# Optimization experiments

Measured on AMD Instinct MI355X. Metric: run time of the kernel, lower is better.

## Reference

```python
import jax, jax.numpy as jnp
import numpy as np
from collections import deque

N, IN_DIM, H, B, L = 512, 64, 128, 256, 2
SOURCE = 105
E_UND = 2048


def _build_graph_and_masks():
    rng = np.random.default_rng(0)
    s = rng.integers(0, N, E_UND)
    d = rng.integers(0, N, E_UND)
    edge_index = np.stack([np.concatenate([s, d]), np.concatenate([d, s])]).astype(np.int32)
    # BFS depths from source (undirected)
    adj = [[] for _ in range(N)]
    for a, b in zip(edge_index[0], edge_index[1]):
        adj[int(a)].append(int(b))
    depths = np.full(N, np.inf)
    depths[SOURCE] = 0.0
    q = deque([SOURCE]); seen = {SOURCE}
    while q:
        u = q.popleft()
        for v in adj[u]:
            if v not in seen:
                seen.add(v); depths[v] = depths[u] + 1.0; q.append(v)
    finite = np.isfinite(depths)
    maxd = depths[finite].max() if finite.any() else 0.0
    depths[~finite] = maxd + 1.0
    adj_mask = np.zeros((N, N), np.float32)
    adj_mask[edge_index[0], edge_index[1]] = 1.0
    adj_mask[edge_index[1], edge_index[0]] = 1.0
    np.fill_diagonal(adj_mask, 1.0)
    direction_mask = (depths[None, :] <= depths[:, None]).astype(np.float32)
    # admittance_matrix is None -> uniform init, then masked
    initial_causal = (np.ones((N, N), np.float32) / N) * adj_mask * direction_mask
    return edge_index, adj_mask, direction_mask, initial_causal


def setup_inputs() -> dict:
    key = jax.random.key(0)
    ks = jax.random.split(key, 16)
    edge_index, adj_mask, direction_mask, initial_causal = _build_graph_and_masks()
    w = lambda k, shp: jax.random.normal(k, shp, jnp.float32) * 0.02
    return {
        'x': jax.random.normal(ks[0], (B, N, IN_DIM), jnp.float32),
        'edge_index': jnp.asarray(edge_index),
        'adj_mask': jnp.asarray(adj_mask),
        'direction_mask': jnp.asarray(direction_mask),
        'causal_logits': jnp.asarray(initial_causal),  # nn.Parameter init
        'W_in': w(ks[1], (IN_DIM, H)), 'b_in': jnp.zeros((H,), jnp.float32),
        'Wq': w(ks[2], (H, H)), 'bq': jnp.zeros((H,), jnp.float32),
        'Wk': w(ks[3], (H, H)), 'bk': jnp.zeros((H,), jnp.float32),
        'Wv': w(ks[4], (H, H)), 'bv': jnp.zeros((H,), jnp.float32),
        'gcn_W': w(ks[5], (L, H, H)), 'gcn_b': jnp.zeros((L, H), jnp.float32),
        'W_fuse': w(ks[6], (2 * H, H)), 'b_fuse': jnp.zeros((H,), jnp.float32),
        'ln_g': jnp.ones((H,), jnp.float32), 'ln_b': jnp.zeros((H,), jnp.float32),
    }


def reference(x, edge_index, adj_mask, direction_mask, causal_logits,
              W_in, b_in, Wq, bq, Wk, bk, Wv, bv,
              gcn_W, gcn_b, W_fuse, b_fuse, ln_g, ln_b):
    n = adj_mask.shape[0]
    h = jax.nn.relu(x @ W_in + b_in)                               # (B,N,H)

    # causal matrix: softmax over learned logits, physically masked, renormalized
    C = jax.nn.softmax(causal_logits, axis=-1) * adj_mask * direction_mask
    C = C / jnp.clip(C.sum(-1, keepdims=True), 1e-8)

    # masked causal attention
    Q = h @ Wq + bq; K = h @ Wk + bk; V = h @ Wv + bv
    scale = jnp.asarray(h.shape[-1] ** 0.5, h.dtype)
    attn = jax.nn.softmax(jnp.einsum('bnh,bmh->bnm', Q, K) / scale, axis=-1)
    attn = attn * C[None]
    attn = attn / (attn.sum(-1, keepdims=True) + 1e-8)
    h_causal = jnp.einsum('bnm,bmh->bnh', attn, V)

    # GCNConv stack (self-loops + symmetric norm; dropout is identity in eval)
    src = jnp.concatenate([edge_index[0], jnp.arange(n, dtype=edge_index.dtype)])
    dst = jnp.concatenate([edge_index[1], jnp.arange(n, dtype=edge_index.dtype)])
    deg = jnp.zeros((n,), h.dtype).at[dst].add(1.0)
    dinv = deg ** -0.5                                              # deg>=1 (self loops)
    norm = (dinv[src] * dinv[dst])[None, :, None]                   # (1,E+N,1)
    h_g = h
    for l in range(gcn_W.shape[0]):
        hW = h_g @ gcn_W[l]                                         # (B,N,H)
        msg = hW[:, src, :] * norm                                  # (B,E+N,H)
        h_g = jnp.zeros_like(hW).at[:, dst, :].add(msg) + gcn_b[l]
        h_g = jax.nn.relu(h_g)

    h_comb = jnp.concatenate([h_causal, h_g], axis=-1) @ W_fuse + b_fuse
    mu = h_comb.mean(-1, keepdims=True)
    var = ((h_comb - mu) ** 2).mean(-1, keepdims=True)
    out = (h_comb - mu) / jnp.sqrt(var + 1e-5) * ln_g + ln_b
    return out, C
```

## Files before the change

### kernel.cpp

```cpp
#include <hip/hip_runtime.h>
#include <hip/hip_bf16.h>
#include <math.h>

#define NN 512
#define HH 128
#define INDIM 64
#define BB 256
#define NE 4096
#define MROWS (BB*NN)
#define OUT0 (BB*NN*HH)

typedef __attribute__((ext_vector_type(8))) short short8v;
typedef __attribute__((ext_vector_type(4))) float float4v;

__device__ __forceinline__ unsigned short f2bf(float f) {
  unsigned u = __float_as_uint(f);
  unsigned r = (u + 0x7fffu + ((u >> 16) & 1u)) >> 16;
  return (unsigned short)r;
}
__device__ __forceinline__ float bf2f(unsigned short b) {
  return __uint_as_float(((unsigned)b) << 16);
}

__global__ __launch_bounds__(256) void k_causalC(
    const float* __restrict__ logits, const float* __restrict__ adj,
    const float* __restrict__ dir, float* __restrict__ Cout)
{
  const int row = blockIdx.x;
  const int t = threadIdx.x;
  __shared__ float red[256];
  const float* lrow = logits + (size_t)row * NN;
  float v0 = lrow[t], v1 = lrow[t + 256];
  float mx = fmaxf(v0, v1);
  red[t] = mx; __syncthreads();
  for (int s = 128; s > 0; s >>= 1) { if (t < s) red[t] = fmaxf(red[t], red[t + s]); __syncthreads(); }
  mx = red[0]; __syncthreads();
  float e0 = __expf(v0 - mx), e1 = __expf(v1 - mx);
  red[t] = e0 + e1; __syncthreads();
  for (int s = 128; s > 0; s >>= 1) { if (t < s) red[t] += red[t + s]; __syncthreads(); }
  float sumE = red[0]; __syncthreads();
  float m0 = adj[(size_t)row * NN + t] * dir[(size_t)row * NN + t];
  float m1 = adj[(size_t)row * NN + t + 256] * dir[(size_t)row * NN + t + 256];
  float me0 = e0 * m0, me1 = e1 * m1;
  red[t] = me0 + me1; __syncthreads();
  for (int s = 128; s > 0; s >>= 1) { if (t < s) red[t] += red[t + s]; __syncthreads(); }
  float sumME = red[0];
  float sm = sumME / sumE;
  float denom = fmaxf(sm, 1e-8f) * sumE;
  Cout[(size_t)row * NN + t]       = me0 / denom;
  Cout[(size_t)row * NN + t + 256] = me1 / denom;
}

__global__ __launch_bounds__(512) void k_csr(const int* __restrict__ ei,
                                             int* __restrict__ rp,
                                             int* __restrict__ ci,
                                             float* __restrict__ cw)
{
  __shared__ int scnt[512];
  __shared__ float sdinv[512];
  __shared__ int sval[512];
  __shared__ int scur[512];
  const int t = threadIdx.x;
  const int* src = ei;
  const int* dst = ei + NE;
  scnt[t] = 0;
  __syncthreads();
  for (int e = t; e < NE; e += 512) atomicAdd(&scnt[dst[e]], 1);
  __syncthreads();
  const int deg = scnt[t] + 1;
  sdinv[t] = rsqrtf((float)deg);
  sval[t] = deg;
  __syncthreads();
  for (int off = 1; off < 512; off <<= 1) {
    int add = (t >= off) ? sval[t - off] : 0;
    __syncthreads();
    sval[t] += add;
    __syncthreads();
  }
  const int excl = sval[t] - deg;
  rp[t] = excl;
  if (t == 511) rp[512] = excl + deg;
  ci[excl] = t;
  cw[excl] = sdinv[t] * sdinv[t];
  scur[t] = excl + 1;
  __syncthreads();
  for (int e = t; e < NE; e += 512) {
    int s = src[e], d = dst[e];
    int p = atomicAdd(&scur[d], 1);
    ci[p] = s;
    cw[p] = sdinv[s] * sdinv[d];
  }
}

__global__ __launch_bounds__(512) void k_ccsr(const int* __restrict__ ei,
                                              const float* __restrict__ Cmat,
                                              int* __restrict__ rp,
                                              int* __restrict__ ci,
                                              float* __restrict__ cw)
{
  __shared__ unsigned bm[512 * 16];
  __shared__ int cnt[512];
  __shared__ int sval[512];
  __shared__ int cur[512];
  const int t = threadIdx.x;
  const int* src = ei;
  const int* dst = ei + NE;
  for (int i = t; i < 512 * 16; i += 512) bm[i] = 0u;
  __syncthreads();
  bm[t * 16 + (t >> 5)] |= (1u << (t & 31));
  cnt[t] = 1;
  __syncthreads();
  for (int e = t; e < NE; e += 512) {
    int r = src[e], c = dst[e];
    if (Cmat[(size_t)r * NN + c] > 0.f) {
      unsigned bit = 1u << (c & 31);
      unsigned old = atomicOr(&bm[r * 16 + (c >> 5)], bit);
      if (!(old & bit)) atomicAdd(&cnt[r], 1);
    }
  }
  __syncthreads();
  const int myc = cnt[t];
  sval[t] = myc;
  __syncthreads();
  for (int off = 1; off < 512; off <<= 1) {
    int add = (t >= off) ? sval[t - off] : 0;
    __syncthreads();
    sval[t] += add;
    __syncthreads();
  }
  const int excl = sval[t] - myc;
  rp[t] = excl;
  if (t == 511) rp[512] = excl + myc;
  ci[excl] = t;
  cw[excl] = Cmat[(size_t)t * NN + t];
  cur[t] = excl + 1;
  bm[t * 16 + (t >> 5)] &= ~(1u << (t & 31));
  __syncthreads();
  for (int e = t; e < NE; e += 512) {
    int r = src[e], c = dst[e];
    if (Cmat[(size_t)r * NN + c] > 0.f) {
      unsigned bit = 1u << (c & 31);
      unsigned old = atomicAnd(&bm[r * 16 + (c >> 5)], ~bit);
      if (old & bit) {
        int p = atomicAdd(&cur[r], 1);
        ci[p] = c;
        cw[p] = Cmat[(size_t)r * NN + c];
      }
    }
  }
}

__global__ __launch_bounds__(256) void k_gcn(
    const unsigned short* __restrict__ hW,
    const int* __restrict__ rp, const int* __restrict__ ci,
    const float* __restrict__ cw, const float* __restrict__ bias,
    unsigned short* __restrict__ out, int OS, int OC0)
{
  const int bid = blockIdx.x;
  const int i5 = bid >> 3;
  const int ng = i5 & 31;
  const int b = (bid & 7) * 32 + (i5 >> 5);
  const int t = threadIdx.x;
  const int node = ng * 16 + (t >> 4);
  const int f0 = (t & 15) * 8;

  float bcol[8];
  #pragma unroll
  for (int k = 0; k < 8; k++) bcol[k] = bias[f0 + k];

  const unsigned short* base = hW + (size_t)b * 512 * 128;
  const int beg = rp[node], end = rp[node + 1];
  float acc[8] = {0.f, 0.f, 0.f, 0.f, 0.f, 0.f, 0.f, 0.f};
  for (int j = beg; j < end; j++) {
    int s = ci[j];
    float w = cw[j];
    short8v v = *(const short8v*)&base[(size_t)s * 128 + f0];
    #pragma unroll
    for (int k = 0; k < 8; k++) acc[k] += w * bf2f((unsigned short)v[k]);
  }
  short8v o;
  #pragma unroll
  for (int k = 0; k < 8; k++) {
    float v = fmaxf(acc[k] + bcol[k], 0.f);
    o[k] = (short)f2bf(v);
  }
  *(short8v*)&out[((size_t)(b * 512 + node)) * OS + OC0 + f0] = o;
}

__global__ __launch_bounds__(256) void k_sattn(
    const unsigned short* __restrict__ Qbf, const unsigned short* __restrict__ Kbf,
    const unsigned short* __restrict__ Vbf,
    const int* __restrict__ rp, const int* __restrict__ ci,
    const float* __restrict__ cw,
    unsigned short* __restrict__ Ocb)
{
  const int bid = blockIdx.x;
  const int i5 = bid >> 3;
  const int ng = i5 & 31;
  const int b = (bid & 7) * 32 + (i5 >> 5);
  const int t = threadIdx.x;
  const int node = ng * 16 + (t >> 4);
  const int f0 = (t & 15) * 8;
  const float scale = 0.088388347648318447f;

  const size_t rowq = ((size_t)(b * 512 + node)) * 128 + f0;
  short8v qv = *(const short8v*)&Qbf[rowq];
  float qf[8];
  #pragma unroll
  for (int k = 0; k < 8; k++) qf[k] = bf2f((unsigned short)qv[k]);

  const unsigned short* Kb = Kbf + (size_t)b * 512 * 128;
  const unsigned short* Vb = Vbf + (size_t)b * 512 * 128;
  const int beg = rp[node], end = rp[node + 1];
  float acc[8] = {0.f, 0.f, 0.f, 0.f, 0.f, 0.f, 0.f, 0.f};
  float sw = 0.f;
  for (int j = beg; j < end; j++) {
    int m = ci[j];
    float w0 = cw[j];
    short8v kv = *(const short8v*)&Kb[(size_t)m * 128 + f0];
    short8v vv = *(const short8v*)&Vb[(size_t)m * 128 + f0];
    float part = 0.f;
    #pragma unroll
    for (int k = 0; k < 8; k++) part += qf[k] * bf2f((unsigned short)kv[k]);
    part += __shfl_xor(part, 1);
    part += __shfl_xor(part, 2);
    part += __shfl_xor(part, 4);
    part += __shfl_xor(part, 8);
    float w = __expf(part * scale) * w0;
    sw += w;
    #pragma unroll
    for (int k = 0; k < 8; k++) acc[k] += w * bf2f((unsigned short)vv[k]);
  }
  float inv = 1.0f / sw;
  short8v o;
  #pragma unroll
  for (int k = 0; k < 8; k++) o[k] = (short)f2bf(acc[k] * inv);
  *(short8v*)&Ocb[((size_t)(b * 512 + node)) * 256 + f0] = o;
}

__global__ __launch_bounds__(256) void k_wt(
    const float* s0, const float* s1, const float* s2, const float* s3,
    const float* s4, const float* s5, const float* s6,
    unsigned short* d0, unsigned short* d1, unsigned short* d2, unsigned short* d3,
    unsigned short* d4, unsigned short* d5, unsigned short* d6)
{
  const float* srcs[7] = {s0, s1, s2, s3, s4, s5, s6};
  unsigned short* dsts[7] = {d0, d1, d2, d3, d4, d5, d6};
  const int Ks[7] = {64, 128, 128, 128, 128, 128, 256};
  const int j = blockIdx.x >> 3;
  const int nc = blockIdx.x & 7;
  const float* s = srcs[j];
  unsigned short* d = dsts[j];
  const int K = Ks[j];
  const int STRW = K + 8;
  const int n0 = nc * 16;
  __shared__ short tile[16 * 264];
  const int t = threadIdx.x;
  for (int i = t; i < K * 16; i += 256) {
    int k = i >> 4, nn = i & 15;
    tile[nn * STRW + k] = (short)f2bf(s[k * 128 + n0 + nn]);
  }
  __syncthreads();
  for (int i = t; i < K * 2; i += 256) {
    int nn = (i * 8) / K;
    int k  = (i * 8) % K;
    *(short8v*)&d[(size_t)(n0 + nn) * K + k] =
        *(const short8v*)&tile[nn * STRW + k];
  }
}

#define GNT 4
template<int KD, bool RELU, bool BATCHW, int OMODE, bool AF32>
__global__ __launch_bounds__(256) void k_bgemm(
    const void* __restrict__ Ap, const unsigned short* __restrict__ Wt,
    const float* __restrict__ bias, void* __restrict__ Out, int OS,
    const float* __restrict__ lng, const float* __restrict__ lnb)
{
  constexpr int KCH = (KD < 128) ? KD : 128;
  constexpr int STR = KCH + 8;
  constexpr bool WONCE = (KD <= 128);
  constexpr int ASH = (64 * STR > 8192) ? 64 * STR : 8192;
  constexpr int TRIPS = KCH / 32;
  __shared__ short lds[ASH + 128 * STR];
  short* As = lds;
  short* Ws = lds + ASH;
  const unsigned short* Abf = (const unsigned short*)Ap;
  const float* Af = (const float*)Ap;
  const int t = threadIdx.x;
  const int wave = t >> 6, lane = t & 63;
  const int l15 = lane & 15, quad = lane >> 4;

  short8v ap[TRIPS];
  float4 fa[TRIPS], fb[TRIPS];

  auto LOADC = [&](int rb, int kc) {
    #pragma unroll
    for (int j = 0; j < TRIPS; j++) {
      int i = t + j * 256;
      int r = i / (KCH / 8), seg = i % (KCH / 8);
      if (AF32) {
        const float* sp = &Af[(size_t)(rb + r) * KD + kc + seg * 8];
        fa[j] = *(const float4*)sp;
        fb[j] = *(const float4*)(sp + 4);
      } else {
        int arow = BATCHW ? ((rb & 511) + r) : (rb + r);
        ap[j] = *(const short8v*)&Abf[(size_t)arow * KD + kc + seg * 8];
      }
    }
  };
  auto STOREC = [&]() {
    #pragma unroll
    for (int j = 0; j < TRIPS; j++) {
      int i = t + j * 256;
      int r = i / (KCH / 8), seg = i % (KCH / 8);
      if (AF32) {
        short8v pk;
        pk[0] = (short)f2bf(fa[j].x); pk[1] = (short)f2bf(fa[j].y);
        pk[2] = (short)f2bf(fa[j].z); pk[3] = (short)f2bf(fa[j].w);
        pk[4] = (short)f2bf(fb[j].x); pk[5] = (short)f2bf(fb[j].y);
        pk[6] = (short)f2bf(fb[j].z); pk[7] = (short)f2bf(fb[j].w);
        *(short8v*)&As[r * STR + seg * 8] = pk;
      } else {
        *(short8v*)&As[r * STR + seg * 8] = ap[j];
      }
    }
  };

  float bcol[8];
  #pragma unroll
  for (int nt = 0; nt < 8; nt++) bcol[nt] = bias ? bias[nt * 16 + l15] : 0.f;
  float gcol[8], bbcol[8];
  if (OMODE == 2) {
    #pragma unroll
    for (int nt = 0; nt < 8; nt++) { gcol[nt] = lng[nt * 16 + l15]; bbcol[nt] = lnb[nt * 16 + l15]; }
  }

  for (int g = blockIdx.x; g < (MROWS / 64) / GNT; g += gridDim.x) {
    if (WONCE) {
      const int b0 = (g * GNT * 64) >> 9;
      const unsigned short* Wb = BATCHW ? (Wt + (size_t)b0 * 128 * KD) : Wt;
      for (int i = t; i < 128 * (KCH / 8); i += 256) {
        int n = i / (KCH / 8), seg = i % (KCH / 8);
        *(short8v*)&Ws[n * STR + seg * 8] =
            *(const short8v*)&Wb[(size_t)n * KD + seg * 8];
      }
    }
    LOADC(g * GNT * 64, 0);
    for (int tt = 0; tt < GNT; tt++) {
      const int tile = g * GNT + tt;
      const int rowbase = tile * 64;
      const int b = rowbase >> 9;
      float4v acc[8];
      #pragma unroll
      for (int nt = 0; nt < 8; nt++) acc[nt] = (float4v){0.f, 0.f, 0.f, 0.f};

      for (int kc = 0; kc < KD; kc += KCH) {
        __syncthreads();
        STOREC();
        if (!WONCE) {
          const unsigned short* Wb = BATCHW ? (Wt + (size_t)b * 128 * KD) : Wt;
          for (int i = t; i < 128 * (KCH / 8); i += 256) {
            int n = i / (KCH / 8), seg = i % (KCH / 8);
            *(short8v*)&Ws[n * STR + seg * 8] =
                *(const short8v*)&Wb[(size_t)n * KD + kc + seg * 8];
          }
        }
        __syncthreads();
        {
          int nkc = kc + KCH, ntt = tt;
          if (nkc >= KD) { nkc = 0; ntt = tt + 1; }
          if (ntt < GNT) LOADC((g * GNT + ntt) * 64, nkc);
        }
        #pragma unroll
        for (int k32 = 0; k32 < KCH / 32; k32++) {
          short8v af = *(const short8v*)&As[(wave * 16 + l15) * STR + k32 * 32 + quad * 8];
          #pragma unroll
          for (int nt = 0; nt < 8; nt++) {
            short8v wf = *(const short8v*)&Ws[(nt * 16 + l15) * STR + k32 * 32 + quad * 8];
            acc[nt] = __builtin_amdgcn_mfma_f32_16x16x32_bf16(af, wf, acc[nt], 0, 0, 0);
          }
        }
      }

      __syncthreads();
      if (OMODE == 0) {
        short* rep = As + wave * 2048;
        #pragma unroll
        for (int nt = 0; nt < 8; nt++)
          #pragma unroll
          for (int r = 0; r < 4; r++) {
            float v = acc[nt][r] + bcol[nt];
            if (RELU) v = fmaxf(v, 0.f);
            rep[(quad * 4 + r) * 128 + nt * 16 + l15] = (short)f2bf(v);
          }
        __syncthreads();
        unsigned short* Ob = (unsigned short*)Out;
        #pragma unroll
        for (int p = 0; p < 4; p++) {
          int row16 = (lane >> 4) + p * 4, seg = lane & 15;
          short8v vv = *(const short8v*)&rep[row16 * 128 + seg * 8];
          *(short8v*)&Ob[(size_t)(rowbase + wave * 16 + row16) * OS + seg * 8] = vv;
        }
      } else if (OMODE == 1) {
        short* rep = As + wave * 2048;
        #pragma unroll
        for (int nt = 0; nt < 8; nt++)
          #pragma unroll
          for (int r = 0; r < 4; r++) {
            float v = acc[nt][r] + bcol[nt];
            if (RELU) v = fmaxf(v, 0.f);
            rep[(nt * 16 + l15) * 16 + quad * 4 + r] = (short)f2bf(v);
          }
        __syncthreads();
        unsigned short* Ob = (unsigned short*)Out;
        int node0 = (rowbase & 511) + wave * 16;
        #pragma unroll
        for (int p = 0; p < 4; p++) {
          int idx = p * 64 + lane, c = idx >> 1, half = idx & 1;
          short8v vv = *(const short8v*)&rep[c * 16 + half * 8];
          *(short8v*)&Ob[((size_t)(b * 128 + c)) * 512 + node0 + half * 8] = vv;
        }
      } else {
        float* repw = (float*)lds + wave * 2048;
        float vv[8][4];
        float s[4] = {0, 0, 0, 0}, ss[4] = {0, 0, 0, 0};
        #pragma unroll
        for (int nt = 0; nt < 8; nt++)
          #pragma unroll
          for (int r = 0; r < 4; r++) {
            float v = acc[nt][r] + bcol[nt];
            vv[nt][r] = v;
            s[r] += v; ss[r] += v * v;
          }
        #pragma unroll
        for (int r = 0; r < 4; r++) {
          s[r] += __shfl_xor(s[r], 1);  s[r] += __shfl_xor(s[r], 2);
          s[r] += __shfl_xor(s[r], 4);  s[r] += __shfl_xor(s[r], 8);
          ss[r] += __shfl_xor(ss[r], 1); ss[r] += __shfl_xor(ss[r], 2);
          ss[r] += __shfl_xor(ss[r], 4); ss[r] += __shfl_xor(ss[r], 8);
        }
        #pragma unroll
        for (int r = 0; r < 4; r++) {
          float mu = s[r] * (1.0f / 128.0f);
          float var = ss[r] * (1.0f / 128.0f) - mu * mu;
          float inv = rsqrtf(var + 1e-5f);
          #pragma unroll
          for (int nt = 0; nt < 8; nt++)
            repw[(quad * 4 + r) * 128 + nt * 16 + l15] =
                (vv[nt][r] - mu) * inv * gcol[nt] + bbcol[nt];
        }
        __syncthreads();
        float* Of = (float*)Out;
        #pragma unroll
        for (int p = 0; p < 8; p++) {
          int row16 = (lane >> 5) + p * 2, seg = lane & 31;
          float4 o = *(const float4*)&repw[row16 * 128 + seg * 4];
          *(float4*)&Of[(size_t)(rowbase + wave * 16 + row16) * 128 + seg * 4] = o;
        }
      }
    }
  }
}

__global__ __launch_bounds__(256) void k_qkv(
    const unsigned short* __restrict__ Abf,
    const unsigned short* __restrict__ W0, const unsigned short* __restrict__ W1,
    const unsigned short* __restrict__ W2,
    const float* __restrict__ b0, const float* __restrict__ b1,
    const float* __restrict__ b2,
    unsigned short* __restrict__ O0, unsigned short* __restrict__ O1,
    unsigned short* __restrict__ O2)
{
  constexpr int STR = 136;
  __shared__ short lds[8704 + 128 * STR];
  short* As = lds;
  short* Ws = lds + 8704;
  const int t = threadIdx.x;
  const int wave = t >> 6, lane = t & 63;
  const int l15 = lane & 15, quad = lane >> 4;

  const unsigned short* Wsrc[3] = {W0, W1, W2};
  const float* Bsrc[3] = {b0, b1, b2};
  unsigned short* Osrc[3] = {O0, O1, O2};

  short8v ap[4];
  auto LOADC = [&](int rb) {
    #pragma unroll
    for (int j = 0; j < 4; j++) {
      int i = t + j * 256;
      int r = i >> 4, seg = i & 15;
      ap[j] = *(const short8v*)&Abf[(size_t)(rb + r) * 128 + seg * 8];
    }
  };

  for (int g = blockIdx.x; g < (MROWS / 64) / GNT; g += gridDim.x) {
    #pragma unroll
    for (int s = 0; s < 3; s++) {
      for (int i = t; i < 128 * 16; i += 256) {
        int n = i >> 4, seg = i & 15;
        *(short8v*)&Ws[n * STR + seg * 8] =
            *(const short8v*)&Wsrc[s][(size_t)n * 128 + seg * 8];
      }
      float bcol[8];
      #pragma unroll
      for (int nt = 0; nt < 8; nt++) bcol[nt] = Bsrc[s][nt * 16 + l15];
      if (s == 0) LOADC(g * GNT * 64);

      for (int tt = 0; tt < GNT; tt++) {
        const int rowbase = (g * GNT + tt) * 64;
        float4v acc[8];
        #pragma unroll
        for (int nt = 0; nt < 8; nt++) acc[nt] = (float4v){0.f, 0.f, 0.f, 0.f};

        __syncthreads();
        #pragma unroll
        for (int j = 0; j < 4; j++) {
          int i = t + j * 256;
          int r = i >> 4, seg = i & 15;
          *(short8v*)&As[r * STR + seg * 8] = ap[j];
        }
        __syncthreads();

        {
          int ntt = tt + 1;
          if (ntt < GNT) LOADC((g * GNT + ntt) * 64);
          else if (s < 2) LOADC(g * GNT * 64);
        }

        #pragma unroll
        for (int k32 = 0; k32 < 4; k32++) {
          short8v af = *(const short8v*)&As[(wave * 16 + l15) * STR + k32 * 32 + quad * 8];
          #pragma unroll
          for (int nt = 0; nt < 8; nt++) {
            short8v wf = *(const short8v*)&Ws[(nt * 16 + l15) * STR + k32 * 32 + quad * 8];
            acc[nt] = __builtin_amdgcn_mfma_f32_16x16x32_bf16(af, wf, acc[nt], 0, 0, 0);
          }
        }
        __syncthreads();

        unsigned short* Ob = Osrc[s];
        short* rep = As + wave * 2048;
        #pragma unroll
        for (int nt = 0; nt < 8; nt++)
          #pragma unroll
          for (int r = 0; r < 4; r++) {
            float v = acc[nt][r] + bcol[nt];
            rep[(quad * 4 + r) * 128 + nt * 16 + l15] = (short)f2bf(v);
          }
        __syncthreads();
        #pragma unroll
        for (int p = 0; p < 4; p++) {
          int row16 = (lane >> 4) + p * 4, seg = lane & 15;
          short8v vv = *(const short8v*)&rep[row16 * 128 + seg * 8];
          *(short8v*)&Ob[(size_t)(rowbase + wave * 16 + row16) * 128 + seg * 8] = vv;
        }
      }
    }
  }
}

extern "C" void kernel_launch(void* const* d_in, const int* in_sizes, int n_in,
                              void* d_out, int out_size, void* d_ws, size_t ws_size,
                              hipStream_t stream)
{
  const float* x     = (const float*)d_in[0];
  const int*   ei    = (const int*)d_in[1];
  const float* adj   = (const float*)d_in[2];
  const float* dmask = (const float*)d_in[3];
  const float* clog  = (const float*)d_in[4];
  const float* W_in  = (const float*)d_in[5];
  const float* b_in  = (const float*)d_in[6];
  const float* Wq    = (const float*)d_in[7];
  const float* bq    = (const float*)d_in[8];
  const float* Wk    = (const float*)d_in[9];
  const float* bk    = (const float*)d_in[10];
  const float* Wv    = (const float*)d_in[11];
  const float* bv    = (const float*)d_in[12];
  const float* gcnW  = (const float*)d_in[13];
  const float* gcnB  = (const float*)d_in[14];
  const float* Wf    = (const float*)d_in[15];
  const float* bf    = (const float*)d_in[16];
  const float* lng   = (const float*)d_in[17];
  const float* lnb   = (const float*)d_in[18];

  float* outp = (float*)d_out;
  float* Cmat = outp + OUT0;

  char* W = (char*)d_ws;
  const size_t SLOT = (size_t)MROWS * 128 * 2;
  unsigned short* A0 = (unsigned short*)(W);
  unsigned short* B0 = (unsigned short*)(W + SLOT);
  unsigned short* C0 = (unsigned short*)(W + 2 * SLOT);
  unsigned short* D0 = (unsigned short*)(W + 3 * SLOT);
  char* AUX = W + 5 * SLOT;
  int*   csr_rp = (int*)AUX;
  int*   csr_ci = csr_rp + 640;
  float* csr_cw = (float*)(csr_ci + 4608);
  int*   crp    = (int*)(AUX + 131072);
  int*   cci    = crp + 640;
  float* ccw    = (float*)(cci + 8192);
  unsigned short* WB    = (unsigned short*)(AUX + 512 * 512 * 4) + 512 * 512 * 2;
  unsigned short* W_int = WB;
  unsigned short* Wqt   = WB + 8192;
  unsigned short* Wkt   = Wqt + 16384;
  unsigned short* Wvt   = Wkt + 16384;
  unsigned short* G0t   = Wvt + 16384;
  unsigned short* G1t   = G0t + 16384;
  unsigned short* Wft   = G1t + 16384;

  unsigned short* Vbf = (unsigned short*)outp;

  k_causalC<<<512, 256, 0, stream>>>(clog, adj, dmask, Cmat);
  k_csr<<<1, 512, 0, stream>>>(ei, csr_rp, csr_ci, csr_cw);
  k_ccsr<<<1, 512, 0, stream>>>(ei, Cmat, crp, cci, ccw);
  k_wt<<<56, 256, 0, stream>>>(W_in, Wq, Wk, Wv, gcnW, gcnW + HH * HH, Wf,
                               W_int, Wqt, Wkt, Wvt, G0t, G1t, Wft);

  k_bgemm<64, true, false, 0, true><<<512, 256, 0, stream>>>(
      x, W_int, b_in, B0, 128, nullptr, nullptr);
  k_bgemm<128, false, false, 0, false><<<512, 256, 0, stream>>>(
      B0, G0t, nullptr, C0, 128, nullptr, nullptr);
  k_gcn<<<8192, 256, 0, stream>>>(C0, csr_rp, csr_ci, csr_cw, gcnB, A0, 128, 0);
  k_bgemm<128, false, false, 0, false><<<512, 256, 0, stream>>>(
      A0, G1t, nullptr, C0, 128, nullptr, nullptr);
  k_gcn<<<8192, 256, 0, stream>>>(C0, csr_rp, csr_ci, csr_cw, gcnB + HH, D0, 256, 128);
  k_qkv<<<512, 256, 0, stream>>>(
      B0, Wqt, Wkt, Wvt, bq, bk, bv, C0, A0, Vbf);
  k_sattn<<<8192, 256, 0, stream>>>(C0, A0, Vbf, crp, cci, ccw, D0);
  k_bgemm<256, false, false, 2, false><<<512, 256, 0, stream>>>(
      D0, Wft, bf, outp, 128, lng, lnb);
}
```

Measured before the change: 388.7 us.

## Fuse GCN aggregation into GEMM by aggregating before transform, prefetch attention neighbors

Each GCN layer previously ran a GEMM followed by a separate sparse aggregation kernel. This uses linearity, A(hW) = (Ah)W, to gather and aggregate neighbor rows straight into LDS as the GEMM A-tile, then apply the MFMA transform with bias and ReLU. That removes one kernel launch and one intermediate round trip per layer. Separately, the sparse attention and the new gather loop software-prefetch the next neighbor's K/V rows. The trade-off is an extra bf16 rounding of the aggregated input, and irregular gathers inside the GEMM kernel may stall the MFMA phase.

After: 566.1 us. 45.7% more time.

```diff
diff --git a/kernel.cpp b/kernel.cpp
--- a/kernel.cpp
+++ b/kernel.cpp
@@ -150,43 +150,6 @@
   }
 }
 
-__global__ __launch_bounds__(256) void k_gcn(
-    const unsigned short* __restrict__ hW,
-    const int* __restrict__ rp, const int* __restrict__ ci,
-    const float* __restrict__ cw, const float* __restrict__ bias,
-    unsigned short* __restrict__ out, int OS, int OC0)
-{
-  const int bid = blockIdx.x;
-  const int i5 = bid >> 3;
-  const int ng = i5 & 31;
-  const int b = (bid & 7) * 32 + (i5 >> 5);
-  const int t = threadIdx.x;
-  const int node = ng * 16 + (t >> 4);
-  const int f0 = (t & 15) * 8;
-
-  float bcol[8];
-  #pragma unroll
-  for (int k = 0; k < 8; k++) bcol[k] = bias[f0 + k];
-
-  const unsigned short* base = hW + (size_t)b * 512 * 128;
-  const int beg = rp[node], end = rp[node + 1];
-  float acc[8] = {0.f, 0.f, 0.f, 0.f, 0.f, 0.f, 0.f, 0.f};
-  for (int j = beg; j < end; j++) {
-    int s = ci[j];
-    float w = cw[j];
-    short8v v = *(const short8v*)&base[(size_t)s * 128 + f0];
-    #pragma unroll
-    for (int k = 0; k < 8; k++) acc[k] += w * bf2f((unsigned short)v[k]);
-  }
-  short8v o;
-  #pragma unroll
-  for (int k = 0; k < 8; k++) {
-    float v = fmaxf(acc[k] + bcol[k], 0.f);
-    o[k] = (short)f2bf(v);
-  }
-  *(short8v*)&out[((size_t)(b * 512 + node)) * OS + OC0 + f0] = o;
-}
-
 __global__ __launch_bounds__(256) void k_sattn(
     const unsigned short* __restrict__ Qbf, const unsigned short* __restrict__ Kbf,
     const unsigned short* __restrict__ Vbf,
@@ -214,11 +177,17 @@
   const int beg = rp[node], end = rp[node + 1];
   float acc[8] = {0.f, 0.f, 0.f, 0.f, 0.f, 0.f, 0.f, 0.f};
   float sw = 0.f;
-  for (int j = beg; j < end; j++) {
-    int m = ci[j];
-    float w0 = cw[j];
-    short8v kv = *(const short8v*)&Kb[(size_t)m * 128 + f0];
-    short8v vv = *(const short8v*)&Vb[(size_t)m * 128 + f0];
+  int j = beg;
+  float w0 = cw[j];
+  int m = ci[j];
+  short8v kv = *(const short8v*)&Kb[(size_t)m * 128 + f0];
+  short8v vv = *(const short8v*)&Vb[(size_t)m * 128 + f0];
+  for (; j < end; ) {
+    const int jn = (j + 1 < end) ? j + 1 : j;
+    const float w02 = cw[jn];
+    const int m2 = ci[jn];
+    short8v kv2 = *(const short8v*)&Kb[(size_t)m2 * 128 + f0];
+    short8v vv2 = *(const short8v*)&Vb[(size_t)m2 * 128 + f0];
     float part = 0.f;
     #pragma unroll
     for (int k = 0; k < 8; k++) part += qf[k] * bf2f((unsigned short)kv[k]);
@@ -230,6 +199,8 @@
     sw += w;
     #pragma unroll
     for (int k = 0; k < 8; k++) acc[k] += w * bf2f((unsigned short)vv[k]);
+    j++;
+    w0 = w02; kv = kv2; vv = vv2;
   }
   float inv = 1.0f / sw;
   short8v o;
@@ -457,6 +428,98 @@
           float4 o = *(const float4*)&repw[row16 * 128 + seg * 4];
           *(float4*)&Of[(size_t)(rowbase + wave * 16 + row16) * 128 + seg * 4] = o;
         }
+      }
+    }
+  }
+}
+
+__global__ __launch_bounds__(256) void k_ggemm(
+    const unsigned short* __restrict__ Abf,
+    const unsigned short* __restrict__ Wt,
+    const int* __restrict__ rp, const int* __restrict__ ci,
+    const float* __restrict__ cw, const float* __restrict__ bias,
+    unsigned short* __restrict__ Out, int OS, int OC0)
+{
+  constexpr int STR = 136;
+  __shared__ short lds[8704 + 128 * STR];
+  short* As = lds;
+  short* Ws = lds + 8704;
+  const int t = threadIdx.x;
+  const int wave = t >> 6, lane = t & 63;
+  const int l15 = lane & 15, quad = lane >> 4;
+
+  for (int i = t; i < 128 * 16; i += 256) {
+    int n = i >> 4, seg = i & 15;
+    *(short8v*)&Ws[n * STR + seg * 8] =
+        *(const short8v*)&Wt[(size_t)n * 128 + seg * 8];
+  }
+  float bcol[8];
+  #pragma unroll
+  for (int nt = 0; nt < 8; nt++) bcol[nt] = bias[nt * 16 + l15];
+
+  for (int g = blockIdx.x; g < (MROWS / 64) / GNT; g += gridDim.x) {
+    for (int tt = 0; tt < GNT; tt++) {
+      const int rowbase = (g * GNT + tt) * 64;
+      const int bbase = rowbase & ~511;
+      const int nb = rowbase & 511;
+      float4v acc[8];
+      #pragma unroll
+      for (int nt = 0; nt < 8; nt++) acc[nt] = (float4v){0.f, 0.f, 0.f, 0.f};
+
+      __syncthreads();
+      #pragma unroll
+      for (int j4 = 0; j4 < 4; j4++) {
+        int i = t + j4 * 256;
+        int r = i >> 4, seg = i & 15;
+        int node = nb + r;
+        int bg = rp[node], en = rp[node + 1];
+        float a8[8] = {0.f, 0.f, 0.f, 0.f, 0.f, 0.f, 0.f, 0.f};
+        int j = bg;
+        float w = cw[j];
+        int m = ci[j];
+        short8v v = *(const short8v*)&Abf[((size_t)(bbase + m)) * 128 + seg * 8];
+        for (; j < en; ) {
+          const int jn = (j + 1 < en) ? j + 1 : j;
+          const float w2 = cw[jn];
+          const int m2 = ci[jn];
+          short8v v2 = *(const short8v*)&Abf[((size_t)(bbase + m2)) * 128 + seg * 8];
+          #pragma unroll
+          for (int k = 0; k < 8; k++) a8[k] += w * bf2f((unsigned short)v[k]);
+          j++;
+          w = w2; v = v2;
+        }
+        short8v pk;
+        #pragma unroll
+        for (int k = 0; k < 8; k++) pk[k] = (short)f2bf(a8[k]);
+        *(short8v*)&As[r * STR + seg * 8] = pk;
+      }
+      __syncthreads();
+
+      #pragma unroll
+      for (int k32 = 0; k32 < 4; k32++) {
+        short8v af = *(const short8v*)&As[(wave * 16 + l15) * STR + k32 * 32 + quad * 8];
+        #pragma unroll
+        for (int nt = 0; nt < 8; nt++) {
+          short8v wf = *(const short8v*)&Ws[(nt * 16 + l15) * STR + k32 * 32 + quad * 8];
+          acc[nt] = __builtin_amdgcn_mfma_f32_16x16x32_bf16(af, wf, acc[nt], 0, 0, 0);
+        }
+      }
+      __syncthreads();
+
+      short* rep = As + wave * 2048;
+      #pragma unroll
+      for (int nt = 0; nt < 8; nt++)
+        #pragma unroll
+        for (int r = 0; r < 4; r++) {
+          float v = fmaxf(acc[nt][r] + bcol[nt], 0.f);
+          rep[(quad * 4 + r) * 128 + nt * 16 + l15] = (short)f2bf(v);
+        }
+      __syncthreads();
+      #pragma unroll
+      for (int p = 0; p < 4; p++) {
+        int row16 = (lane >> 4) + p * 4, seg = lane & 15;
+        short8v vv = *(const short8v*)&rep[row16 * 128 + seg * 8];
+        *(short8v*)&Out[(size_t)(rowbase + wave * 16 + row16) * OS + OC0 + seg * 8] = vv;
       }
     }
   }
@@ -618,12 +681,10 @@
 
   k_bgemm<64, true, false, 0, true><<<512, 256, 0, stream>>>(
       x, W_int, b_in, B0, 128, nullptr, nullptr);
-  k_bgemm<128, false, false, 0, false><<<512, 256, 0, stream>>>(
-      B0, G0t, nullptr, C0, 128, nullptr, nullptr);
-  k_gcn<<<8192, 256, 0, stream>>>(C0, csr_rp, csr_ci, csr_cw, gcnB, A0, 128, 0);
-  k_bgemm<128, false, false, 0, false><<<512, 256, 0, stream>>>(
-      A0, G1t, nullptr, C0, 128, nullptr, nullptr);
-  k_gcn<<<8192, 256, 0, stream>>>(C0, csr_rp, csr_ci, csr_cw, gcnB + HH, D0, 256, 128);
+  k_ggemm<<<512, 256, 0, stream>>>(
+      B0, G0t, csr_rp, csr_ci, csr_cw, gcnB, A0, 128, 0);
+  k_ggemm<<<512, 256, 0, stream>>>(
+      A0, G1t, csr_rp, csr_ci, csr_cw, gcnB + HH, D0, 256, 128);
   k_qkv<<<512, 256, 0, stream>>>(
       B0, Wqt, Wkt, Wvt, bq, bk, bv, C0, A0, Vbf);
   k_sattn<<<8192, 256, 0, stream>>>(C0, A0, Vbf, crp, cci, ccw, D0);
```

## Fuse first GCN projection into QKV GEMM and merge second GCN with sparse attention

Applied to the files above, without the earlier changes.

The QKV projection kernel now also computes the first GCN weight product from the same input tile, so the input activations are read once for four projections and one GEMM launch goes away. The second GCN aggregation and the sparse causal attention now run in a single launch with 16384 blocks, split by block index, which removes a launch boundary and lets both gather workloads overlap. The attention neighbor loop also prefetches the next neighbor's K/V rows one iteration ahead to hide gather latency. In exchange it needs an extra K buffer carved from the output region and more registers in the attention loop.

Result: no change. 392.8 us (+1.1%).

```diff
diff --git a/kernel.cpp b/kernel.cpp
--- a/kernel.cpp
+++ b/kernel.cpp
@@ -150,13 +150,12 @@
   }
 }
 
-__global__ __launch_bounds__(256) void k_gcn(
-    const unsigned short* __restrict__ hW,
+__device__ __forceinline__ void gcn_body(
+    int bid, const unsigned short* __restrict__ hW,
     const int* __restrict__ rp, const int* __restrict__ ci,
     const float* __restrict__ cw, const float* __restrict__ bias,
     unsigned short* __restrict__ out, int OS, int OC0)
 {
-  const int bid = blockIdx.x;
   const int i5 = bid >> 3;
   const int ng = i5 & 31;
   const int b = (bid & 7) * 32 + (i5 >> 5);
@@ -187,14 +186,21 @@
   *(short8v*)&out[((size_t)(b * 512 + node)) * OS + OC0 + f0] = o;
 }
 
-__global__ __launch_bounds__(256) void k_sattn(
-    const unsigned short* __restrict__ Qbf, const unsigned short* __restrict__ Kbf,
-    const unsigned short* __restrict__ Vbf,
+__global__ __launch_bounds__(256) void k_gcn(
+    const unsigned short* __restrict__ hW,
     const int* __restrict__ rp, const int* __restrict__ ci,
-    const float* __restrict__ cw,
-    unsigned short* __restrict__ Ocb)
-{
-  const int bid = blockIdx.x;
+    const float* __restrict__ cw, const float* __restrict__ bias,
+    unsigned short* __restrict__ out, int OS, int OC0)
+{
+  gcn_body(blockIdx.x, hW, rp, ci, cw, bias, out, OS, OC0);
+}
+
+__device__ __forceinline__ void sattn_body(
+    int bid, const unsigned short* __restrict__ Qbf,
+    const unsigned short* __restrict__ Kbf, const unsigned short* __restrict__ Vbf,
+    const int* __restrict__ rp, const int* __restrict__ ci,
+    const float* __restrict__ cw, unsigned short* __restrict__ Ocb)
+{
   const int i5 = bid >> 3;
   const int ng = i5 & 31;
   const int b = (bid & 7) * 32 + (i5 >> 5);
@@ -214,11 +220,17 @@
   const int beg = rp[node], end = rp[node + 1];
   float acc[8] = {0.f, 0.f, 0.f, 0.f, 0.f, 0.f, 0.f, 0.f};
   float sw = 0.f;
-  for (int j = beg; j < end; j++) {
-    int m = ci[j];
-    float w0 = cw[j];
-    short8v kv = *(const short8v*)&Kb[(size_t)m * 128 + f0];
-    short8v vv = *(const short8v*)&Vb[(size_t)m * 128 + f0];
+  int j = beg;
+  float w0 = cw[j];
+  int m = ci[j];
+  short8v kv = *(const short8v*)&Kb[(size_t)m * 128 + f0];
+  short8v vv = *(const short8v*)&Vb[(size_t)m * 128 + f0];
+  for (; j < end; ) {
+    const int jn = (j + 1 < end) ? j + 1 : j;
+    const float w02 = cw[jn];
+    const int m2 = ci[jn];
+    short8v kv2 = *(const short8v*)&Kb[(size_t)m2 * 128 + f0];
+    short8v vv2 = *(const short8v*)&Vb[(size_t)m2 * 128 + f0];
     float part = 0.f;
     #pragma unroll
     for (int k = 0; k < 8; k++) part += qf[k] * bf2f((unsigned short)kv[k]);
@@ -230,12 +242,30 @@
     sw += w;
     #pragma unroll
     for (int k = 0; k < 8; k++) acc[k] += w * bf2f((unsigned short)vv[k]);
+    j++;
+    w0 = w02; kv = kv2; vv = vv2;
   }
   float inv = 1.0f / sw;
   short8v o;
   #pragma unroll
   for (int k = 0; k < 8; k++) o[k] = (short)f2bf(acc[k] * inv);
   *(short8v*)&Ocb[((size_t)(b * 512 + node)) * 256 + f0] = o;
+}
+
+__global__ __launch_bounds__(256) void k_gs(
+    const unsigned short* __restrict__ hW,
+    const int* __restrict__ grp, const int* __restrict__ gci,
+    const float* __restrict__ gcw, const float* __restrict__ gbias,
+    const unsigned short* __restrict__ Qbf, const unsigned short* __restrict__ Kbf,
+    const unsigned short* __restrict__ Vbf,
+    const int* __restrict__ arp, const int* __restrict__ aci,
+    const float* __restrict__ acw,
+    unsigned short* __restrict__ Dout)
+{
+  if (blockIdx.x < 8192)
+    gcn_body(blockIdx.x, hW, grp, gci, gcw, gbias, Dout, 256, 128);
+  else
+    sattn_body(blockIdx.x - 8192, Qbf, Kbf, Vbf, arp, aci, acw, Dout);
 }
 
 __global__ __launch_bounds__(256) void k_wt(
@@ -462,14 +492,14 @@
   }
 }
 
-__global__ __launch_bounds__(256) void k_qkv(
+__global__ __launch_bounds__(256) void k_qkv4(
     const unsigned short* __restrict__ Abf,
     const unsigned short* __restrict__ W0, const unsigned short* __restrict__ W1,
-    const unsigned short* __restrict__ W2,
-    const float* __restrict__ b0, const float* __restrict__ b1,
-    const float* __restrict__ b2,
+    const unsigned short* __restrict__ W2, const unsigned short* __restrict__ W3,
+    const float* __restrict__ b1, const float* __restrict__ b2,
+    const float* __restrict__ b3,
     unsigned short* __restrict__ O0, unsigned short* __restrict__ O1,
-    unsigned short* __restrict__ O2)
+    unsigned short* __restrict__ O2, unsigned short* __restrict__ O3)
 {
   constexpr int STR = 136;
   __shared__ short lds[8704 + 128 * STR];
@@ -479,9 +509,9 @@
   const int wave = t >> 6, lane = t & 63;
   const int l15 = lane & 15, quad = lane >> 4;
 
-  const unsigned short* Wsrc[3] = {W0, W1, W2};
-  const float* Bsrc[3] = {b0, b1, b2};
-  unsigned short* Osrc[3] = {O0, O1, O2};
+  const unsigned short* Wsrc[4] = {W0, W1, W2, W3};
+  const float* Bsrc[4] = {nullptr, b1, b2, b3};
+  unsigned short* Osrc[4] = {O0, O1, O2, O3};
 
   short8v ap[4];
   auto LOADC = [&](int rb) {
@@ -495,7 +525,7 @@
 
   for (int g = blockIdx.x; g < (MROWS / 64) / GNT; g += gridDim.x) {
     #pragma unroll
-    for (int s = 0; s < 3; s++) {
+    for (int s = 0; s < 4; s++) {
       for (int i = t; i < 128 * 16; i += 256) {
         int n = i >> 4, seg = i & 15;
         *(short8v*)&Ws[n * STR + seg * 8] =
@@ -503,7 +533,7 @@
       }
       float bcol[8];
       #pragma unroll
-      for (int nt = 0; nt < 8; nt++) bcol[nt] = Bsrc[s][nt * 16 + l15];
+      for (int nt = 0; nt < 8; nt++) bcol[nt] = Bsrc[s] ? Bsrc[s][nt * 16 + l15] : 0.f;
       if (s == 0) LOADC(g * GNT * 64);
 
       for (int tt = 0; tt < GNT; tt++) {
@@ -524,7 +554,7 @@
         {
           int ntt = tt + 1;
           if (ntt < GNT) LOADC((g * GNT + ntt) * 64);
-          else if (s < 2) LOADC(g * GNT * 64);
+          else if (s < 3) LOADC(g * GNT * 64);
         }
 
         #pragma unroll
@@ -609,6 +639,7 @@
   unsigned short* Wft   = G1t + 16384;
 
   unsigned short* Vbf = (unsigned short*)outp;
+  unsigned short* E0  = Vbf + (size_t)MROWS * 128;
 
   k_causalC<<<512, 256, 0, stream>>>(clog, adj, dmask, Cmat);
   k_csr<<<1, 512, 0, stream>>>(ei, csr_rp, csr_ci, csr_cw);
@@ -618,15 +649,14 @@
 
   k_bgemm<64, true, false, 0, true><<<512, 256, 0, stream>>>(
       x, W_int, b_in, B0, 128, nullptr, nullptr);
+  k_qkv4<<<512, 256, 0, stream>>>(
+      B0, G0t, Wqt, Wkt, Wvt, bq, bk, bv, A0, C0, E0, Vbf);
+  k_gcn<<<8192, 256, 0, stream>>>(A0, csr_rp, csr_ci, csr_cw, gcnB, B0, 128, 0);
   k_bgemm<128, false, false, 0, false><<<512, 256, 0, stream>>>(
-      B0, G0t, nullptr, C0, 128, nullptr, nullptr);
-  k_gcn<<<8192, 256, 0, stream>>>(C0, csr_rp, csr_ci, csr_cw, gcnB, A0, 128, 0);
-  k_bgemm<128, false, false, 0, false><<<512, 256, 0, stream>>>(
-      A0, G1t, nullptr, C0, 128, nullptr, nullptr);
-  k_gcn<<<8192, 256, 0, stream>>>(C0, csr_rp, csr_ci, csr_cw, gcnB + HH, D0, 256, 128);
-  k_qkv<<<512, 256, 0, stream>>>(
-      B0, Wqt, Wkt, Wvt, bq, bk, bv, C0, A0, Vbf);
-  k_sattn<<<8192, 256, 0, stream>>>(C0, A0, Vbf, crp, cci, ccw, D0);
+      B0, G1t, nullptr, A0, 128, nullptr, nullptr);
+  k_gs<<<16384, 256, 0, stream>>>(
+      A0, csr_rp, csr_ci, csr_cw, gcnB + HH,
+      C0, E0, Vbf, crp, cci, ccw, D0);
   k_bgemm<256, false, false, 2, false><<<512, 256, 0, stream>>>(
       D0, Wft, bf, outp, 128, lng, lnb);
 }
```
